# Performance work log

Hardware: AMD Instinct MI355X
Metric: run time of the kernel (lower is better)

## Reference

```python
import jax, jax.numpy as jnp
import numpy as np

N_NODES = 50000
N_EDGES = 600000
IN_FEAT = 128
EDGE_DIM = 3
N_HEADS = 4
OUT_FEAT = 32  # per head; N_HEADS*OUT_FEAT == IN_FEAT -> residual_proj is Identity


def setup_inputs() -> dict:
    key = jax.random.key(0)
    ks = jax.random.split(key, 16)
    s = 0.05
    H, F = N_HEADS, OUT_FEAT
    return {
        "node_feats": jax.random.normal(ks[0], (N_NODES, IN_FEAT), jnp.float32),
        "edge_feat": jax.random.normal(ks[1], (N_EDGES, EDGE_DIM), jnp.float32),
        "src": jax.random.randint(ks[2], (N_EDGES,), 0, N_NODES),
        "dst": jax.random.randint(ks[3], (N_EDGES,), 0, N_NODES),
        "W_em1": jax.random.normal(ks[4], (EDGE_DIM, 2 * EDGE_DIM), jnp.float32) * s,
        "b_em1": jnp.zeros((2 * EDGE_DIM,), jnp.float32),
        "W_em2": jax.random.normal(ks[5], (2 * EDGE_DIM, EDGE_DIM), jnp.float32) * s,
        "b_em2": jnp.zeros((EDGE_DIM,), jnp.float32),
        "W_np": jax.random.normal(ks[6], (IN_FEAT, IN_FEAT), jnp.float32) * s,
        "b_np": jnp.zeros((IN_FEAT,), jnp.float32),
        "W_fc": jax.random.normal(ks[7], (IN_FEAT + EDGE_DIM, H * F), jnp.float32) * s,
        "attn_l": jax.random.normal(ks[8], (H, F), jnp.float32) * s,
        "attn_r": jax.random.normal(ks[9], (H, F), jnp.float32) * s,
        "gat_bias": jnp.zeros((H * F,), jnp.float32),
        "ln_gamma": jnp.ones((H * F,), jnp.float32),
        "ln_beta": jnp.zeros((H * F,), jnp.float32),
    }


def reference(node_feats, edge_feat, src, dst, W_em1, b_em1, W_em2, b_em2,
              W_np, b_np, W_fc, attn_l, attn_r, gat_bias, ln_gamma, ln_beta):
    N = node_feats.shape[0]
    H, F = attn_l.shape
    # edge MLP: Linear -> SiLU -> Linear
    e = jax.nn.silu(edge_feat @ W_em1 + b_em1) @ W_em2 + b_em2            # [E, ED]
    p = node_feats @ W_np + b_np                                          # [N, IN]
    src_in = jnp.concatenate([p[src], e], axis=1)                         # [E, IN+ED]
    dst_in = jnp.concatenate([p[dst], e], axis=1)                         # [E, IN+ED]
    temp = jnp.zeros((N, src_in.shape[1]), node_feats.dtype)
    temp = temp.at[src].add(src_in).at[dst].add(dst_in)                   # scatter_add x2
    # GATConv (eval mode: feat_drop/attn_drop are identity)
    h = (temp @ W_fc).reshape(N, H, F)                                    # [N, H, F]
    el = jnp.einsum('nhf,hf->nh', h, attn_l)                              # [N, H]
    er = jnp.einsum('nhf,hf->nh', h, attn_r)                              # [N, H]
    logits = jax.nn.leaky_relu(el[src] + er[dst], negative_slope=0.2)     # [E, H]
    # destination-wise edge softmax (stable)
    m = jax.ops.segment_max(logits, dst, num_segments=N)                  # [N, H]
    a = jnp.exp(logits - m[dst])                                          # [E, H]
    z = jax.ops.segment_sum(a, dst, num_segments=N)                       # [N, H]
    alpha = a / z[dst]                                                    # [E, H]
    msg = alpha[:, :, None] * h[src]                                      # [E, H, F]
    rst = jax.ops.segment_sum(msg, dst, num_segments=N)                   # [N, H, F]
    rst = rst + gat_bias.reshape(1, H, F)
    gat_out = rst.reshape(N, H * F)
    out = gat_out + node_feats                                            # residual (Identity proj)
    mu = out.mean(axis=-1, keepdims=True)
    var = out.var(axis=-1, keepdims=True)
    out = (out - mu) / jnp.sqrt(var + 1e-5) * ln_gamma + ln_beta          # LayerNorm
    return jax.nn.silu(out)
```

## Files before the change

### kernel.cpp

```cpp
#include <hip/hip_runtime.h>
#include <hip/hip_bf16.h>

#define IN_FEAT 128
#define N_HEADS 4
#define OUT_FEAT 32

typedef __attribute__((ext_vector_type(8))) short short8;
typedef __attribute__((ext_vector_type(4))) float floatx4;

__device__ __forceinline__ void bf16split(float x, short& hi, short& lo) {
    unsigned u = __float_as_uint(x);
    unsigned r = (u + 0x7FFFu + ((u >> 16) & 1u)) & 0xFFFF0000u;
    hi = (short)(r >> 16);
    float res = x - __uint_as_float(r);
    unsigned u2 = __float_as_uint(res);
    unsigned r2 = u2 + 0x7FFFu + ((u2 >> 16) & 1u);
    lo = (short)(r2 >> 16);
}

__device__ __forceinline__ unsigned short bf16rne(float x) {
    unsigned u = __float_as_uint(x);
    return (unsigned short)((u + 0x7FFFu + ((u >> 16) & 1u)) >> 16);
}

__global__ void edge_scatter_kernel(const float* __restrict__ ef,
                                    const int* __restrict__ src, const int* __restrict__ dst,
                                    const float* __restrict__ W1, const float* __restrict__ b1,
                                    const float* __restrict__ W2, const float* __restrict__ b2,
                                    float* __restrict__ nd, int* __restrict__ erank, int E) {
    int t = blockIdx.x * blockDim.x + threadIdx.x;
    int e = t >> 3;
    int sub = t & 7;
    if (e >= E) return;
    float x0 = ef[e * 3 + 0], x1 = ef[e * 3 + 1], x2 = ef[e * 3 + 2];
    float hbuf[6];
#pragma unroll
    for (int j = 0; j < 6; j++) {
        float v = x0 * W1[0 * 6 + j] + x1 * W1[1 * 6 + j] + x2 * W1[2 * 6 + j] + b1[j];
        hbuf[j] = v / (1.0f + __expf(-v));
    }
    int j = sub & 3;
    float val;
    if (j == 0) {
        val = 1.0f;
    } else {
        float v = b2[j - 1];
#pragma unroll
        for (int k = 0; k < 6; k++) v += hbuf[k] * W2[k * 3 + (j - 1)];
        val = v;
    }
    int side = sub >> 2;
    int node = side ? dst[e] : src[e];
    int slot = (side && j == 0) ? 4 : j;
    float old = atomicAdd(&nd[(size_t)node * 8 + slot], val);
    if (sub == 4) erank[e] = (int)old;
}

__global__ __launch_bounds__(1024) void scan1_kernel(const float* __restrict__ nd,
                                                     int* __restrict__ excl,
                                                     int* __restrict__ bsum, int N) {
    __shared__ int buf[1024];
    int t = threadIdx.x;
    int i = blockIdx.x * 1024 + t;
    int v = (i < N) ? (int)nd[(size_t)i * 8 + 4] : 0;
    buf[t] = v;
    __syncthreads();
    for (int d = 1; d < 1024; d <<= 1) {
        int x = (t >= d) ? buf[t - d] : 0;
        __syncthreads();
        buf[t] += x;
        __syncthreads();
    }
    if (i < N) excl[i] = buf[t] - v;
    if (t == 1023) bsum[blockIdx.x] = buf[1023];
}

__global__ __launch_bounds__(1024) void scan3_kernel(const int* __restrict__ excl,
                                                     const int* __restrict__ bsum,
                                                     int* __restrict__ off, int N, int E) {
    __shared__ int base;
    if (threadIdx.x == 0) {
        int s = 0;
        for (int k = 0; k < (int)blockIdx.x; k++) s += bsum[k];
        base = s;
    }
    __syncthreads();
    int i = blockIdx.x * 1024 + threadIdx.x;
    if (i < N) off[i] = excl[i] + base;
    if (i == 0) off[N] = E;
}

__global__ void wcomb_kernel(const float* __restrict__ W_np, const float* __restrict__ W_fc,
                             const float* __restrict__ b_np,
                             short* __restrict__ WBh, short* __restrict__ WBl,
                             float* __restrict__ bvec,
                             float4* __restrict__ ndz, int zcnt) {
    for (int i = blockIdx.x * blockDim.x + threadIdx.x; i < zcnt; i += gridDim.x * blockDim.x)
        ndz[i] = (float4){0.f, 0.f, 0.f, 0.f};

    int i = blockIdx.x;
    int o = threadIdx.x;
    float acc = 0.0f;
    for (int j = 0; j < 128; j++) acc += W_np[i * 128 + j] * W_fc[j * 128 + o];
    short hi, lo;
    bf16split(acc, hi, lo);
    int t    = o >> 4;
    int kk   = i >> 5;
    int lane = ((i >> 3) & 3) * 16 + (o & 15);
    int jj   = i & 7;
    int fi = ((t * 4 + kk) * 64 + lane) * 8 + jj;
    WBh[fi] = hi;
    WBl[fi] = lo;
    if (i == 0) {
        float bb = 0.0f;
        for (int j = 0; j < 128; j++) bb += b_np[j] * W_fc[j * 128 + o];
        bvec[o] = bb;
    }
}

__global__ __launch_bounds__(256) void binh_kernel(
        const int* __restrict__ src, const int* __restrict__ dst,
        const int* __restrict__ eoff, const int* __restrict__ erank,
        int* __restrict__ ssrc, int E,
        const float* __restrict__ nf,
        const short* __restrict__ WBh, const short* __restrict__ WBl,
        const float* __restrict__ bvec, const float* __restrict__ W_fc,
        const float* __restrict__ nd,
        const float* __restrict__ attn_l, const float* __restrict__ attn_r,
        unsigned short* __restrict__ h16,
        float* __restrict__ el, float* __restrict__ er, int N) {
    {
        int stride = gridDim.x * 256;
        for (int e = blockIdx.x * 256 + threadIdx.x; e < E; e += stride) {
            ssrc[eoff[dst[e]] + erank[e]] = src[e];
        }
    }

    const int w = threadIdx.x >> 6, l = threadIdx.x & 63;
    const int lrow = l & 15, lhalf = l >> 4;
    const int n0 = blockIdx.x * 64 + w * 16;
    const int arow = n0 + lrow;

    short8 ah[4];
#pragma unroll
    for (int kk = 0; kk < 4; kk++) {
        float v[8];
        if (arow < N) {
            const float* p = &nf[(size_t)arow * 128 + kk * 32 + lhalf * 8];
            float4 f0 = *(const float4*)p;
            float4 f1 = *(const float4*)(p + 4);
            v[0] = f0.x; v[1] = f0.y; v[2] = f0.z; v[3] = f0.w;
            v[4] = f1.x; v[5] = f1.y; v[6] = f1.z; v[7] = f1.w;
        } else {
#pragma unroll
            for (int j = 0; j < 8; j++) v[j] = 0.0f;
        }
#pragma unroll
        for (int j = 0; j < 8; j++) ah[kk][j] = (short)bf16rne(v[j]);
    }

    const short8* gbh = (const short8*)WBh;
    const short8* gbl = (const short8*)WBl;
    floatx4 acc[8];
#pragma unroll
    for (int t = 0; t < 8; t++) acc[t] = (floatx4){0.f, 0.f, 0.f, 0.f};
#pragma unroll
    for (int t = 0; t < 8; t++) {
#pragma unroll
        for (int kk = 0; kk < 4; kk++) {
            short8 bh = gbh[(t * 4 + kk) * 64 + l];
            short8 bl = gbl[(t * 4 + kk) * 64 + l];
            acc[t] = __builtin_amdgcn_mfma_f32_16x16x32_bf16(ah[kk], bh, acc[t], 0, 0, 0);
            acc[t] = __builtin_amdgcn_mfma_f32_16x16x32_bf16(ah[kk], bl, acc[t], 0, 0, 0);
        }
    }

    float bv[8], w0[8], w1[8], w2[8], alb[8], arb[8];
#pragma unroll
    for (int t = 0; t < 8; t++) {
        int o = t * 16 + lrow;
        bv[t] = bvec[o];
        w0[t] = W_fc[128 * 128 + o];
        w1[t] = W_fc[129 * 128 + o];
        w2[t] = W_fc[130 * 128 + o];
        alb[t] = attn_l[o];
        arb[t] = attn_r[o];
    }
#pragma unroll
    for (int r = 0; r < 4; r++) {
        int node = n0 + lhalf * 4 + r;
        bool valid = node < N;
        float dg = 0.f, e0 = 0.f, e1 = 0.f, e2 = 0.f;
        if (valid) {
            dg = nd[(size_t)node * 8 + 0] + nd[(size_t)node * 8 + 4];
            e0 = nd[(size_t)node * 8 + 1];
            e1 = nd[(size_t)node * 8 + 2];
            e2 = nd[(size_t)node * 8 + 3];
        }
        float pl[4] = {0.f, 0.f, 0.f, 0.f}, pr[4] = {0.f, 0.f, 0.f, 0.f};
#pragma unroll
        for (int t = 0; t < 8; t++) {
            float hv = dg * (acc[t][r] + bv[t]) + e0 * w0[t] + e1 * w1[t] + e2 * w2[t];
            if (valid) h16[(size_t)node * 128 + t * 16 + lrow] = bf16rne(hv);
            pl[t >> 1] += hv * alb[t];
            pr[t >> 1] += hv * arb[t];
        }
#pragma unroll
        for (int hd = 0; hd < 4; hd++) {
#pragma unroll
            for (int mask = 1; mask <= 8; mask <<= 1) {
                pl[hd] += __shfl_xor(pl[hd], mask);
                pr[hd] += __shfl_xor(pr[hd], mask);
            }
        }
        if (valid) {
            if (lrow < 4)      el[node * 4 + lrow]       = pl[lrow];
            else if (lrow < 8) er[node * 4 + (lrow - 4)] = pr[lrow - 4];
        }
    }
}

__global__ __launch_bounds__(256) void gather_kernel(
        const int* __restrict__ off, const int* __restrict__ sorted_src,
        const float* __restrict__ el, const float* __restrict__ er,
        const unsigned short* __restrict__ h16, const float* __restrict__ nf,
        const float* __restrict__ gat_bias, const float* __restrict__ gamma,
        const float* __restrict__ beta, float* __restrict__ out, int N) {
    int wid  = (blockIdx.x * blockDim.x + threadIdx.x) >> 6;
    int lane = threadIdx.x & 63;
    int half = lane >> 5;
    int li   = lane & 31;
    int n = wid * 2 + half;
    if (n >= N) return;
    int o0 = li * 4;
    int hd = li >> 3;
    float ern = er[(unsigned)(n * 4 + hd)];
    int beg = off[n], end = off[n + 1];
    float z = 0.f, a0 = 0.f, a1 = 0.f, a2 = 0.f, a3 = 0.f;
    if (beg < end) {
        int s = sorted_src[beg];
        float elv = el[(unsigned)(s * 4 + hd)];
        uint2 hb = *(const uint2*)&h16[(unsigned)(s * 128 + o0)];
        for (int j = beg; j < end; j++) {
            int s2 = (j + 1 < end) ? sorted_src[j + 1] : s;
            float elv2 = el[(unsigned)(s2 * 4 + hd)];
            uint2 hb2 = *(const uint2*)&h16[(unsigned)(s2 * 128 + o0)];
            float l = elv + ern;
            l = (l > 0.f) ? l : 0.2f * l;
            float p = __expf(l);
            z  += p;
            a0 += p * __uint_as_float(hb.x << 16);
            a1 += p * __uint_as_float(hb.x & 0xFFFF0000u);
            a2 += p * __uint_as_float(hb.y << 16);
            a3 += p * __uint_as_float(hb.y & 0xFFFF0000u);
            elv = elv2; hb = hb2; s = s2;
        }
    }
    float izv = (end > beg) ? 1.0f / z : 0.f;
    float4 nfv = *(const float4*)&nf[(size_t)n * 128 + o0];
    float v0 = a0 * izv + gat_bias[o0]     + nfv.x;
    float v1 = a1 * izv + gat_bias[o0 + 1] + nfv.y;
    float v2 = a2 * izv + gat_bias[o0 + 2] + nfv.z;
    float v3 = a3 * izv + gat_bias[o0 + 3] + nfv.w;
    float s  = v0 + v1 + v2 + v3;
    float s2 = v0 * v0 + v1 * v1 + v2 * v2 + v3 * v3;
#pragma unroll
    for (int mask = 1; mask <= 16; mask <<= 1) {
        s  += __shfl_xor(s, mask);
        s2 += __shfl_xor(s2, mask);
    }
    float mu = s * (1.0f / 128.0f);
    float var = s2 * (1.0f / 128.0f) - mu * mu;
    float inv = rsqrtf(var + 1e-5f);
    float y0 = (v0 - mu) * inv * gamma[o0]     + beta[o0];
    float y1 = (v1 - mu) * inv * gamma[o0 + 1] + beta[o0 + 1];
    float y2 = (v2 - mu) * inv * gamma[o0 + 2] + beta[o0 + 2];
    float y3 = (v3 - mu) * inv * gamma[o0 + 3] + beta[o0 + 3];
    float4 ov;
    ov.x = y0 / (1.0f + __expf(-y0));
    ov.y = y1 / (1.0f + __expf(-y1));
    ov.z = y2 / (1.0f + __expf(-y2));
    ov.w = y3 / (1.0f + __expf(-y3));
    *(float4*)&out[(size_t)n * 128 + o0] = ov;
}

extern "C" void kernel_launch(void* const* d_in, const int* in_sizes, int n_in,
                              void* d_out, int out_size, void* d_ws, size_t ws_size,
                              hipStream_t stream) {
    const float* nf     = (const float*)d_in[0];
    const float* ef     = (const float*)d_in[1];
    const int*   src    = (const int*)d_in[2];
    const int*   dst    = (const int*)d_in[3];
    const float* W_em1  = (const float*)d_in[4];
    const float* b_em1  = (const float*)d_in[5];
    const float* W_em2  = (const float*)d_in[6];
    const float* b_em2  = (const float*)d_in[7];
    const float* W_np   = (const float*)d_in[8];
    const float* b_np   = (const float*)d_in[9];
    const float* W_fc   = (const float*)d_in[10];
    const float* attn_l = (const float*)d_in[11];
    const float* attn_r = (const float*)d_in[12];
    const float* g_bias = (const float*)d_in[13];
    const float* ln_g   = (const float*)d_in[14];
    const float* ln_b   = (const float*)d_in[15];

    const int N = in_sizes[0] / IN_FEAT;
    const int E = in_sizes[2];

    float* ws = (float*)d_ws;
    size_t off_w = 0;
    auto alloc = [&](size_t nelem) {
        float* p = ws + off_w;
        off_w += (nelem + 63) & ~(size_t)63;
        return p;
    };
    float* nd    = alloc((size_t)N * 8);
    short* WBh   = (short*)alloc(128 * 128 / 2);
    short* WBl   = (short*)alloc(128 * 128 / 2);
    float* bvec  = alloc(128);
    unsigned short* h16 = (unsigned short*)alloc((size_t)N * 64);
    float* el    = alloc((size_t)N * 4);
    float* er    = alloc((size_t)N * 4);
    int*   erank  = (int*)alloc(E);
    int*   eoff   = (int*)alloc(N + 1);
    int*   ssrc   = (int*)alloc(E);
    int*   excl   = (int*)alloc(N);
    int*   bsum   = (int*)alloc(1024);

    const int nb = (N + 1023) / 1024;

    wcomb_kernel<<<128, 128, 0, stream>>>(W_np, W_fc, b_np, WBh, WBl, bvec,
                                          (float4*)nd, N * 2);
    edge_scatter_kernel<<<((size_t)E * 8 + 255) / 256, 256, 0, stream>>>(
        ef, src, dst, W_em1, b_em1, W_em2, b_em2, nd, erank, E);
    scan1_kernel<<<nb, 1024, 0, stream>>>(nd, excl, bsum, N);
    scan3_kernel<<<nb, 1024, 0, stream>>>(excl, bsum, eoff, N, E);
    binh_kernel<<<(N + 63) / 64, 256, 0, stream>>>(src, dst, eoff, erank, ssrc, E,
                                                   nf, WBh, WBl, bvec, W_fc, nd,
                                                   attn_l, attn_r, h16, el, er, N);
    gather_kernel<<<((size_t)N * 32 + 255) / 256, 256, 0, stream>>>(eoff, ssrc, el, er, h16, nf,
                                                                    g_bias, ln_g, ln_b,
                                                                    (float*)d_out, N);
}
```

Measured before the change: 151.4 us.

## Stage fused weight matrix in LDS and unroll gather loop by two

The binh kernel now copies the split bf16 hi/lo weight tiles (64 KB total) into shared memory once per block and reads MFMA B operands from LDS instead of global memory. The gather kernel's edge loop is restructured from a software-prefetch form into a two-edge unrolled loop with an odd-count prologue, so more independent loads are in flight per iteration. The 64 KB LDS footprint per block limits how many blocks fit per CU and adds a copy plus barrier per block, which may cost more than the L2-cached global reads it replaces.

Result: no change. 148.5 us, median of 2 (-1.9%).

```diff
diff --git a/kernel.cpp b/kernel.cpp
--- a/kernel.cpp
+++ b/kernel.cpp
@@ -129,6 +129,17 @@
         const float* __restrict__ attn_l, const float* __restrict__ attn_r,
         unsigned short* __restrict__ h16,
         float* __restrict__ el, float* __restrict__ er, int N) {
+    __shared__ short lWh[16384];
+    __shared__ short lWl[16384];
+    {
+        const int4* s1 = (const int4*)WBh;
+        const int4* s2 = (const int4*)WBl;
+        int4* d1 = (int4*)lWh;
+        int4* d2 = (int4*)lWl;
+        for (int i = threadIdx.x; i < 2048; i += 256) { d1[i] = s1[i]; d2[i] = s2[i]; }
+    }
+    __syncthreads();
+
     {
         int stride = gridDim.x * 256;
         for (int e = blockIdx.x * 256 + threadIdx.x; e < E; e += stride) {
@@ -159,8 +170,6 @@
         for (int j = 0; j < 8; j++) ah[kk][j] = (short)bf16rne(v[j]);
     }
 
-    const short8* gbh = (const short8*)WBh;
-    const short8* gbl = (const short8*)WBl;
     floatx4 acc[8];
 #pragma unroll
     for (int t = 0; t < 8; t++) acc[t] = (floatx4){0.f, 0.f, 0.f, 0.f};
@@ -168,8 +177,9 @@
     for (int t = 0; t < 8; t++) {
 #pragma unroll
         for (int kk = 0; kk < 4; kk++) {
-            short8 bh = gbh[(t * 4 + kk) * 64 + l];
-            short8 bl = gbl[(t * 4 + kk) * 64 + l];
+            int fi = ((t * 4 + kk) * 64 + l) * 8;
+            short8 bh = *(const short8*)&lWh[fi];
+            short8 bl = *(const short8*)&lWl[fi];
             acc[t] = __builtin_amdgcn_mfma_f32_16x16x32_bf16(ah[kk], bh, acc[t], 0, 0, 0);
             acc[t] = __builtin_amdgcn_mfma_f32_16x16x32_bf16(ah[kk], bl, acc[t], 0, 0, 0);
         }
@@ -237,24 +247,35 @@
     float ern = er[(unsigned)(n * 4 + hd)];
     int beg = off[n], end = off[n + 1];
     float z = 0.f, a0 = 0.f, a1 = 0.f, a2 = 0.f, a3 = 0.f;
-    if (beg < end) {
-        int s = sorted_src[beg];
-        float elv = el[(unsigned)(s * 4 + hd)];
+    int j = beg;
+    if ((end - beg) & 1) {
+        int s = sorted_src[j++];
+        float l = el[(unsigned)(s * 4 + hd)] + ern;
+        l = (l > 0.f) ? l : 0.2f * l;
+        float p = __expf(l);
         uint2 hb = *(const uint2*)&h16[(unsigned)(s * 128 + o0)];
-        for (int j = beg; j < end; j++) {
-            int s2 = (j + 1 < end) ? sorted_src[j + 1] : s;
-            float elv2 = el[(unsigned)(s2 * 4 + hd)];
-            uint2 hb2 = *(const uint2*)&h16[(unsigned)(s2 * 128 + o0)];
-            float l = elv + ern;
-            l = (l > 0.f) ? l : 0.2f * l;
-            float p = __expf(l);
-            z  += p;
-            a0 += p * __uint_as_float(hb.x << 16);
-            a1 += p * __uint_as_float(hb.x & 0xFFFF0000u);
-            a2 += p * __uint_as_float(hb.y << 16);
-            a3 += p * __uint_as_float(hb.y & 0xFFFF0000u);
-            elv = elv2; hb = hb2; s = s2;
-        }
+        z  = p;
+        a0 = p * __uint_as_float(hb.x << 16);
+        a1 = p * __uint_as_float(hb.x & 0xFFFF0000u);
+        a2 = p * __uint_as_float(hb.y << 16);
+        a3 = p * __uint_as_float(hb.y & 0xFFFF0000u);
+    }
+    for (; j < end; j += 2) {
+        int sA = sorted_src[j];
+        int sB = sorted_src[j + 1];
+        float elA = el[(unsigned)(sA * 4 + hd)];
+        float elB = el[(unsigned)(sB * 4 + hd)];
+        uint2 hA = *(const uint2*)&h16[(unsigned)(sA * 128 + o0)];
+        uint2 hB = *(const uint2*)&h16[(unsigned)(sB * 128 + o0)];
+        float lA = elA + ern; lA = (lA > 0.f) ? lA : 0.2f * lA;
+        float lB = elB + ern; lB = (lB > 0.f) ? lB : 0.2f * lB;
+        float pA = __expf(lA);
+        float pB = __expf(lB);
+        z  += pA + pB;
+        a0 += pA * __uint_as_float(hA.x << 16)         + pB * __uint_as_float(hB.x << 16);
+        a1 += pA * __uint_as_float(hA.x & 0xFFFF0000u) + pB * __uint_as_float(hB.x & 0xFFFF0000u);
+        a2 += pA * __uint_as_float(hA.y << 16)         + pB * __uint_as_float(hB.y << 16);
+        a3 += pA * __uint_as_float(hA.y & 0xFFFF0000u) + pB * __uint_as_float(hB.y & 0xFFFF0000u);
     }
     float izv = (end > beg) ? 1.0f / z : 0.f;
     float4 nfv = *(const float4*)&nf[(size_t)n * 128 + o0];
```
